# Performance work log

Hardware: AMD Instinct MI355X
Metric: run time of the kernel (lower is better)

Reference implementation:

```python
import jax, jax.numpy as jnp
import numpy as np

B, IN_DIM, OUT_DIM = 4096, 2048, 2048
EMA_M = 0.95
LN_EPS = 1e-5


def setup_inputs() -> dict:
    key = jax.random.key(0)
    ks = jax.random.split(key, 8)
    x = jax.random.normal(ks[0], (B, IN_DIM), dtype=jnp.float32)
    # W_slow is orthogonal-init in torch (gain 0.5); scaled gaussian is a fine stand-in for math testing
    W_slow = jax.random.normal(ks[1], (OUT_DIM, IN_DIM), dtype=jnp.float32) * (0.5 / np.sqrt(IN_DIM))
    # buffers start at zero in torch; use small nonzero values so the medium/fast GEMMs are exercised
    W_medium = jax.random.normal(ks[2], (OUT_DIM, IN_DIM), dtype=jnp.float32) * 0.01
    W_fast = jax.random.normal(ks[3], (OUT_DIM, IN_DIM), dtype=jnp.float32) * 0.01
    ln_gamma = jnp.ones((OUT_DIM,), jnp.float32) + 0.1 * jax.random.normal(ks[4], (OUT_DIM,), dtype=jnp.float32)
    ln_beta = 0.1 * jax.random.normal(ks[5], (OUT_DIM,), dtype=jnp.float32)
    pc_w1 = jax.random.normal(ks[6], (8, 3), dtype=jnp.float32) * 0.5
    pc_b1 = jnp.zeros((8,), jnp.float32)
    pc_w2 = jax.random.normal(ks[7], (1, 8), dtype=jnp.float32) * 0.5
    pc_b2 = jnp.full((1,), -1.5, jnp.float32)  # torch fills last Linear bias with -1.5
    ema_mean = jnp.zeros((1,), jnp.float32)
    ema_std = jnp.ones((1,), jnp.float32)
    return {"x": x, "W_slow": W_slow, "W_medium": W_medium, "W_fast": W_fast,
            "ln_gamma": ln_gamma, "ln_beta": ln_beta,
            "pc_w1": pc_w1, "pc_b1": pc_b1, "pc_w2": pc_w2, "pc_b2": pc_b2,
            "ema_mean": ema_mean, "ema_std": ema_std}


def reference(x, W_slow, W_medium, W_fast, ln_gamma, ln_beta,
              pc_w1, pc_b1, pc_w2, pc_b2, ema_mean, ema_std):
    xc = jnp.clip(x, -5.0, 5.0)
    slow_out = jnp.clip(xc @ W_slow.T, -10.0, 10.0)
    pre_act = jnp.clip(slow_out + xc @ W_medium.T + xc @ W_fast.T, -10.0, 10.0)  # [B, OUT]

    batch_mean = pre_act.mean(axis=1, keepdims=True)                      # [B,1]
    batch_std = jnp.maximum(pre_act.std(axis=1, keepdims=True), 1e-6)     # [B,1], ddof=0

    # EMA buffer update (no-grad in torch); clamps applied after update
    new_mean = jnp.clip(EMA_M * ema_mean + (1.0 - EMA_M) * batch_mean.mean(), -0.5, 0.5)
    new_std = jnp.clip(EMA_M * ema_std + (1.0 - EMA_M) * batch_std.mean(), 0.1, 1.5)
    homeostasis = new_std / (jnp.abs(new_mean) + 1e-6)                    # [1]

    stats = jnp.concatenate([batch_mean, batch_std,
                             jnp.broadcast_to(homeostasis[None, :], (batch_mean.shape[0], 1))], axis=1)  # [B,3]
    h = jax.nn.gelu(stats @ pc_w1.T + pc_b1, approximate=False)           # torch GELU is exact erf
    learned_plasticity = jax.nn.sigmoid(h @ pc_w2.T + pc_b2)[:, 0]        # [B] (does not affect `out`)
    _ = learned_plasticity  # kept for fidelity with original compute graph

    # LayerNorm over last dim, eps=1e-5
    mu = pre_act.mean(axis=-1, keepdims=True)
    var = pre_act.var(axis=-1, keepdims=True)
    normed = (pre_act - mu) * jax.lax.rsqrt(var + LN_EPS) * ln_gamma + ln_beta
    out = 5.0 * jnp.tanh(normed / 5.0)
    return out
```

## Files before the change

### kernel.cpp

```cpp
#include <hip/hip_runtime.h>
#include <hip/hip_bf16.h>

#define BDIM    4096
#define IN_DIM  2048
#define OUT_DIM 2048

typedef __attribute__((ext_vector_type(4))) float  floatx4;
typedef __attribute__((ext_vector_type(8))) short  bf16x8;

__device__ __forceinline__ unsigned short f2bf(float f) {
    union { float f; unsigned u; } v; v.f = f;
    unsigned r = v.u + 0x7FFFu + ((v.u >> 16) & 1u);
    return (unsigned short)(r >> 16);
}

__device__ __forceinline__ void async16(const unsigned short* g, unsigned short* l) {
    __builtin_amdgcn_global_load_lds(
        (const __attribute__((address_space(1))) unsigned int*)g,
        (__attribute__((address_space(3))) unsigned int*)l,
        16, 0, 0);
}

__global__ __launch_bounds__(256) void prep(const float* __restrict__ x,
                                            const float* __restrict__ Ws,
                                            const float* __restrict__ Wm,
                                            const float* __restrict__ Wf,
                                            unsigned short* __restrict__ xc,
                                            unsigned short* __restrict__ bsum) {
    int b = blockIdx.x;
    if (b < 8192) {
        int i = b * 256 + threadIdx.x;
        float4 v = ((const float4*)x)[i];
        ushort4 o;
        o.x = f2bf(fminf(fmaxf(v.x, -5.f), 5.f));
        o.y = f2bf(fminf(fmaxf(v.y, -5.f), 5.f));
        o.z = f2bf(fminf(fmaxf(v.z, -5.f), 5.f));
        o.w = f2bf(fminf(fmaxf(v.w, -5.f), 5.f));
        ((ushort4*)xc)[i] = o;
    } else {
        int i = (b - 8192) * 256 + threadIdx.x;
        float4 s = ((const float4*)Ws)[i];
        float4 m = ((const float4*)Wm)[i];
        float4 f = ((const float4*)Wf)[i];
        ushort4 o;
        o.x = f2bf(s.x + m.x + f.x);
        o.y = f2bf(s.y + m.y + f.y);
        o.z = f2bf(s.z + m.z + f.z);
        o.w = f2bf(s.w + m.w + f.w);
        ((ushort4*)bsum)[i] = o;
    }
}

#define TILE   128
#define BK     64
#define KSPLIT 2
#define KHALF  (IN_DIM / KSPLIT)

__global__ __launch_bounds__(256) void gemm_bt(const unsigned short* __restrict__ A,
                                               const unsigned short* __restrict__ B,
                                               float* __restrict__ Cpart) {
    constexpr int N = OUT_DIM, K = IN_DIM;
    __shared__ __align__(16) unsigned short As[TILE * BK];
    __shared__ __align__(16) unsigned short Bs[TILE * BK];

    const int tid  = threadIdx.x;
    const int lane = tid & 63;
    const int wave = tid >> 6;
    const int wm   = (wave >> 1) * 64;
    const int wn   = (wave & 1) * 64;
    const int rowBlock = blockIdx.y * TILE;
    const int colBlock = blockIdx.x * TILE;
    const int kBase    = blockIdx.z * KHALF;
    float* C = Cpart + (size_t)blockIdx.z * BDIM * OUT_DIM;

    const int sRow = tid >> 3;
    const int sSeg = (tid & 7) ^ (sRow & 7);
    const unsigned short* aSrc = A + (size_t)(rowBlock + sRow) * K + kBase + sSeg * 8;
    const unsigned short* bSrc = B + (size_t)(colBlock + sRow) * K + kBase + sSeg * 8;
    unsigned short* AsDst = As + tid * 8;
    unsigned short* BsDst = Bs + tid * 8;

    floatx4 acc[4][4] = {};

    const int fragRow = lane & 15;
    const int quad    = lane >> 4;
    const int l7      = lane & 7;

    for (int k0 = 0; k0 < KHALF; k0 += BK) {
#pragma unroll
        for (int r = 0; r < 4; r++)
            async16(aSrc + k0 + (size_t)(r * 32) * K, AsDst + r * 32 * BK);
#pragma unroll
        for (int r = 0; r < 4; r++)
            async16(bSrc + k0 + (size_t)(r * 32) * K, BsDst + r * 32 * BK);
        __syncthreads();

#pragma unroll
        for (int kk = 0; kk < 2; kk++) {
            const int xs = ((quad + kk * 4) ^ l7) << 3;
            bf16x8 af[4], bfr[4];
#pragma unroll
            for (int i = 0; i < 4; i++) {
                af[i]  = *(const bf16x8*)(As + (wm + i * 16 + fragRow) * BK + xs);
                bfr[i] = *(const bf16x8*)(Bs + (wn + i * 16 + fragRow) * BK + xs);
            }
#pragma unroll
            for (int i = 0; i < 4; i++)
#pragma unroll
                for (int j = 0; j < 4; j++)
                    acc[i][j] = __builtin_amdgcn_mfma_f32_16x16x32_bf16(af[i], bfr[j], acc[i][j], 0, 0, 0);
        }
        __syncthreads();
    }

    const int cCol = colBlock + wn + (lane & 15);
    const int cRow = rowBlock + wm + (lane >> 4) * 4;
#pragma unroll
    for (int i = 0; i < 4; i++) {
#pragma unroll
        for (int j = 0; j < 4; j++) {
            const int col = cCol + j * 16;
            const int rb  = cRow + i * 16;
#pragma unroll
            for (int r = 0; r < 4; r++)
                C[(size_t)(rb + r) * N + col] = acc[i][j][r];
        }
    }
}

__global__ __launch_bounds__(256) void ln_kernel(const float* __restrict__ Cpart,
                                                 const float* __restrict__ gamma,
                                                 const float* __restrict__ beta,
                                                 float* __restrict__ out) {
    const int row = blockIdx.x;
    const int tid = threadIdx.x;
    __shared__ float wsum[4], wsq[4];

    const float4* Ca = (const float4*)(Cpart + (size_t)row * OUT_DIM);
    const float4* Cb = (const float4*)(Cpart + (size_t)BDIM * OUT_DIM + (size_t)row * OUT_DIM);

    float4 p[2];
    float sum = 0.f, sq = 0.f;
#pragma unroll
    for (int it = 0; it < 2; it++) {
        int i = tid + it * 256;
        float4 a = Ca[i];
        float4 b = Cb[i];
        float4 q;
        q.x = fminf(fmaxf(a.x + b.x, -10.f), 10.f);
        q.y = fminf(fmaxf(a.y + b.y, -10.f), 10.f);
        q.z = fminf(fmaxf(a.z + b.z, -10.f), 10.f);
        q.w = fminf(fmaxf(a.w + b.w, -10.f), 10.f);
        p[it] = q;
        sum += q.x + q.y + q.z + q.w;
        sq  += q.x * q.x + q.y * q.y + q.z * q.z + q.w * q.w;
    }
#pragma unroll
    for (int off = 32; off > 0; off >>= 1) {
        sum += __shfl_down(sum, off);
        sq  += __shfl_down(sq,  off);
    }
    if ((tid & 63) == 0) { wsum[tid >> 6] = sum; wsq[tid >> 6] = sq; }
    __syncthreads();
    const float tsum = wsum[0] + wsum[1] + wsum[2] + wsum[3];
    const float tsq  = wsq[0]  + wsq[1]  + wsq[2]  + wsq[3];
    const float mu   = tsum * (1.0f / OUT_DIM);
    const float var  = tsq * (1.0f / OUT_DIM) - mu * mu;
    const float inv  = rsqrtf(var + 1e-5f);

#pragma unroll
    for (int it = 0; it < 2; it++) {
        int i = tid + it * 256;
        float4 q = p[it];
        float4 g = *(const float4*)(gamma + i * 4);
        float4 b = *(const float4*)(beta + i * 4);
        float4 o;
        float zx = (q.x - mu) * inv * g.x + b.x;
        float zy = (q.y - mu) * inv * g.y + b.y;
        float zz = (q.z - mu) * inv * g.z + b.z;
        float zw = (q.w - mu) * inv * g.w + b.w;
        o.x = 5.f * (1.f - 2.f / (__expf(0.4f * zx) + 1.f));
        o.y = 5.f * (1.f - 2.f / (__expf(0.4f * zy) + 1.f));
        o.z = 5.f * (1.f - 2.f / (__expf(0.4f * zz) + 1.f));
        o.w = 5.f * (1.f - 2.f / (__expf(0.4f * zw) + 1.f));
        *(float4*)(out + (size_t)row * OUT_DIM + i * 4) = o;
    }
}

extern "C" void kernel_launch(void* const* d_in, const int* in_sizes, int n_in,
                              void* d_out, int out_size, void* d_ws, size_t ws_size,
                              hipStream_t stream) {
    const float* x     = (const float*)d_in[0];
    const float* Ws    = (const float*)d_in[1];
    const float* Wm    = (const float*)d_in[2];
    const float* Wf    = (const float*)d_in[3];
    const float* gamma = (const float*)d_in[4];
    const float* beta  = (const float*)d_in[5];
    float* out = (float*)d_out;

    char* ws = (char*)d_ws;
    unsigned short* xc   = (unsigned short*)ws;
    unsigned short* bsum = (unsigned short*)(ws + (size_t)16 * 1024 * 1024);
    float*          Cbuf = (float*)(ws + (size_t)24 * 1024 * 1024);

    prep<<<12288, 256, 0, stream>>>(x, Ws, Wm, Wf, xc, bsum);
    dim3 g(OUT_DIM / TILE, BDIM / TILE, KSPLIT);
    gemm_bt<<<g, 256, 0, stream>>>(xc, bsum, Cbuf);
    ln_kernel<<<BDIM, 256, 0, stream>>>(Cbuf, gamma, beta, out);
}
```

Baseline: 204.2 us.

## Drop split-K, double-buffer LDS tiles, store bf16 GEMM output

```diff
diff --git a/kernel.cpp b/kernel.cpp
--- a/kernel.cpp
+++ b/kernel.cpp
@@ -12,6 +12,11 @@
     union { float f; unsigned u; } v; v.f = f;
     unsigned r = v.u + 0x7FFFu + ((v.u >> 16) & 1u);
     return (unsigned short)(r >> 16);
+}
+
+__device__ __forceinline__ float bf2f(unsigned short h) {
+    union { unsigned u; float f; } v; v.u = (unsigned)h << 16;
+    return v.f;
 }
 
 __device__ __forceinline__ void async16(const unsigned short* g, unsigned short* l) {
@@ -51,17 +56,18 @@
     }
 }
 
-#define TILE   128
-#define BK     64
-#define KSPLIT 2
-#define KHALF  (IN_DIM / KSPLIT)
-
-__global__ __launch_bounds__(256) void gemm_bt(const unsigned short* __restrict__ A,
-                                               const unsigned short* __restrict__ B,
-                                               float* __restrict__ Cpart) {
+#define TILE  128
+#define BK    64
+#define ITERS (IN_DIM / BK)
+
+#define MEMBAR() asm volatile("" ::: "memory")
+
+__global__ __launch_bounds__(256, 2) void gemm_bt(const unsigned short* __restrict__ A,
+                                                  const unsigned short* __restrict__ B,
+                                                  unsigned short* __restrict__ C) {
     constexpr int N = OUT_DIM, K = IN_DIM;
-    __shared__ __align__(16) unsigned short As[TILE * BK];
-    __shared__ __align__(16) unsigned short Bs[TILE * BK];
+    __shared__ __align__(16) unsigned short As[2 * TILE * BK];
+    __shared__ __align__(16) unsigned short Bs[2 * TILE * BK];
 
     const int tid  = threadIdx.x;
     const int lane = tid & 63;
@@ -70,15 +76,11 @@
     const int wn   = (wave & 1) * 64;
     const int rowBlock = blockIdx.y * TILE;
     const int colBlock = blockIdx.x * TILE;
-    const int kBase    = blockIdx.z * KHALF;
-    float* C = Cpart + (size_t)blockIdx.z * BDIM * OUT_DIM;
 
     const int sRow = tid >> 3;
     const int sSeg = (tid & 7) ^ (sRow & 7);
-    const unsigned short* aSrc = A + (size_t)(rowBlock + sRow) * K + kBase + sSeg * 8;
-    const unsigned short* bSrc = B + (size_t)(colBlock + sRow) * K + kBase + sSeg * 8;
-    unsigned short* AsDst = As + tid * 8;
-    unsigned short* BsDst = Bs + tid * 8;
+    const unsigned short* aSrc = A + (size_t)(rowBlock + sRow) * K + sSeg * 8;
+    const unsigned short* bSrc = B + (size_t)(colBlock + sRow) * K + sSeg * 8;
 
     floatx4 acc[4][4] = {};
 
@@ -86,14 +88,30 @@
     const int quad    = lane >> 4;
     const int l7      = lane & 7;
 
-    for (int k0 = 0; k0 < KHALF; k0 += BK) {
+    auto stage = [&](int t, int p) {
+        unsigned short* ad = As + p * TILE * BK + tid * 8;
+        unsigned short* bd = Bs + p * TILE * BK + tid * 8;
+        const unsigned short* ag = aSrc + t * BK;
+        const unsigned short* bg = bSrc + t * BK;
 #pragma unroll
         for (int r = 0; r < 4; r++)
-            async16(aSrc + k0 + (size_t)(r * 32) * K, AsDst + r * 32 * BK);
+            async16(ag + (size_t)(r * 32) * K, ad + r * 32 * BK);
 #pragma unroll
         for (int r = 0; r < 4; r++)
-            async16(bSrc + k0 + (size_t)(r * 32) * K, BsDst + r * 32 * BK);
-        __syncthreads();
+            async16(bg + (size_t)(r * 32) * K, bd + r * 32 * BK);
+    };
+
+    stage(0, 0);
+    stage(1, 1);
+    __builtin_amdgcn_s_waitcnt(0xF78);
+    MEMBAR();
+    __builtin_amdgcn_s_barrier();
+    MEMBAR();
+
+    for (int k = 0; k < ITERS; k++) {
+        const int p = k & 1;
+        const unsigned short* Ab = As + p * TILE * BK;
+        const unsigned short* Bb = Bs + p * TILE * BK;
 
 #pragma unroll
         for (int kk = 0; kk < 2; kk++) {
@@ -101,8 +119,8 @@
             bf16x8 af[4], bfr[4];
 #pragma unroll
             for (int i = 0; i < 4; i++) {
-                af[i]  = *(const bf16x8*)(As + (wm + i * 16 + fragRow) * BK + xs);
-                bfr[i] = *(const bf16x8*)(Bs + (wn + i * 16 + fragRow) * BK + xs);
+                af[i]  = *(const bf16x8*)(Ab + (wm + i * 16 + fragRow) * BK + xs);
+                bfr[i] = *(const bf16x8*)(Bb + (wn + i * 16 + fragRow) * BK + xs);
             }
 #pragma unroll
             for (int i = 0; i < 4; i++)
@@ -110,7 +128,19 @@
                 for (int j = 0; j < 4; j++)
                     acc[i][j] = __builtin_amdgcn_mfma_f32_16x16x32_bf16(af[i], bfr[j], acc[i][j], 0, 0, 0);
         }
-        __syncthreads();
+
+        MEMBAR();
+        __builtin_amdgcn_s_barrier();
+        MEMBAR();
+        if (k < ITERS - 2) {
+            stage(k + 2, p);
+            __builtin_amdgcn_s_waitcnt(0xF78);
+        } else {
+            __builtin_amdgcn_s_waitcnt(0xF70);
+        }
+        MEMBAR();
+        __builtin_amdgcn_s_barrier();
+        MEMBAR();
     }
 
     const int cCol = colBlock + wn + (lane & 15);
@@ -123,12 +153,12 @@
             const int rb  = cRow + i * 16;
 #pragma unroll
             for (int r = 0; r < 4; r++)
-                C[(size_t)(rb + r) * N + col] = acc[i][j][r];
+                C[(size_t)(rb + r) * N + col] = f2bf(acc[i][j][r]);
         }
     }
 }
 
-__global__ __launch_bounds__(256) void ln_kernel(const float* __restrict__ Cpart,
+__global__ __launch_bounds__(256) void ln_kernel(const unsigned short* __restrict__ C,
                                                  const float* __restrict__ gamma,
                                                  const float* __restrict__ beta,
                                                  float* __restrict__ out) {
@@ -136,21 +166,22 @@
     const int tid = threadIdx.x;
     __shared__ float wsum[4], wsq[4];
 
-    const float4* Ca = (const float4*)(Cpart + (size_t)row * OUT_DIM);
-    const float4* Cb = (const float4*)(Cpart + (size_t)BDIM * OUT_DIM + (size_t)row * OUT_DIM);
+    const uint2* Cr = (const uint2*)(C + (size_t)row * OUT_DIM);
 
     float4 p[2];
     float sum = 0.f, sq = 0.f;
 #pragma unroll
     for (int it = 0; it < 2; it++) {
-        int i = tid + it * 256;
-        float4 a = Ca[i];
-        float4 b = Cb[i];
+        uint2 u = Cr[tid + it * 256];
         float4 q;
-        q.x = fminf(fmaxf(a.x + b.x, -10.f), 10.f);
-        q.y = fminf(fmaxf(a.y + b.y, -10.f), 10.f);
-        q.z = fminf(fmaxf(a.z + b.z, -10.f), 10.f);
-        q.w = fminf(fmaxf(a.w + b.w, -10.f), 10.f);
+        q.x = bf2f((unsigned short)(u.x & 0xFFFF));
+        q.y = bf2f((unsigned short)(u.x >> 16));
+        q.z = bf2f((unsigned short)(u.y & 0xFFFF));
+        q.w = bf2f((unsigned short)(u.y >> 16));
+        q.x = fminf(fmaxf(q.x, -10.f), 10.f);
+        q.y = fminf(fmaxf(q.y, -10.f), 10.f);
+        q.z = fminf(fmaxf(q.z, -10.f), 10.f);
+        q.w = fminf(fmaxf(q.w, -10.f), 10.f);
         p[it] = q;
         sum += q.x + q.y + q.z + q.w;
         sq  += q.x * q.x + q.y * q.y + q.z * q.z + q.w * q.w;
@@ -201,10 +232,10 @@
     char* ws = (char*)d_ws;
     unsigned short* xc   = (unsigned short*)ws;
     unsigned short* bsum = (unsigned short*)(ws + (size_t)16 * 1024 * 1024);
-    float*          Cbuf = (float*)(ws + (size_t)24 * 1024 * 1024);
+    unsigned short* Cbuf = (unsigned short*)(ws + (size_t)24 * 1024 * 1024);
 
     prep<<<12288, 256, 0, stream>>>(x, Ws, Wm, Wf, xc, bsum);
-    dim3 g(OUT_DIM / TILE, BDIM / TILE, KSPLIT);
+    dim3 g(OUT_DIM / TILE, BDIM / TILE);
     gemm_bt<<<g, 256, 0, stream>>>(xc, bsum, Cbuf);
     ln_kernel<<<BDIM, 256, 0, stream>>>(Cbuf, gamma, beta, out);
 }
```

Result: faster. 181.7 us (-11.0%).
